# Performance work log

Measured on AMD Instinct MI355X. Metric: run time of the kernel, lower is better.

Reference implementation:

```python
import jax, jax.numpy as jnp
import numpy as np

BS = 8
LOW_RATIO = 0.25
HIGH_RATIO = 0.25


def _dct_matrix(n: int) -> np.ndarray:
    # DCT-II orthonormal matrix, row k = sqrt(2/n)*cos(pi*k*(2i+1)/(2n)), row 0 = 1/sqrt(n)
    k = np.arange(n)[:, None].astype(np.float64)
    i = np.arange(n)[None, :].astype(np.float64)
    D = np.sqrt(2.0 / n) * np.cos(np.pi * k * (2 * i + 1) / (2 * n))
    D[0, :] = 1.0 / np.sqrt(n)
    return D.astype(np.float32)


def _zigzag_indices(n: int) -> np.ndarray:
    idx = np.zeros((n, n), dtype=np.int64)
    i = j = 0
    for c in range(n * n):
        idx[i, j] = c
        if (i + j) % 2 == 0:
            if j == n - 1:
                i += 1
            elif i == 0:
                j += 1
            else:
                i -= 1; j += 1
        elif i == n - 1:
            j += 1
        elif j == 0:
            i += 1
        else:
            i += 1; j -= 1
    return idx


def _band_masks(n: int) -> np.ndarray:
    z = _zigzag_indices(n)
    total = n * n
    lo_thr = int(total * LOW_RATIO)        # 16 for n=8
    hi_thr = int(total * (1 - HIGH_RATIO)) # 48 for n=8
    low = (z < lo_thr)
    high = (z >= hi_thr)
    mid = ~(low | high)
    return np.stack([low, mid, high]).astype(np.float32)  # [3, n, n]


def setup_inputs() -> dict:
    key = jax.random.key(0)
    x = jax.random.normal(key, (32, 3, 512, 512), dtype=jnp.float32)
    return {"x": x}


def reference(x) -> jnp.ndarray:
    # Frequency decomposition: blocked 8x8 DCT -> band masking -> blocked IDCT.
    # Returns stacked (low, mid, high) bands: [3, B, C, H, W].
    D = jnp.asarray(_dct_matrix(BS))          # [bs, bs]
    M = jnp.asarray(_band_masks(BS))          # [3, bs, bs]
    B, C, H, W = x.shape
    Hb, Wb = H // BS, W // BS                 # H, W divisible by BS (no padding path)
    # blockify: [B, C, Hb, Wb, bs, bs]
    xb = x.reshape(B, C, Hb, BS, Wb, BS).transpose(0, 1, 2, 4, 3, 5)
    # forward block DCT: D @ block @ D^T
    coef = jnp.einsum('ki,bcuvij,lj->bcuvkl', D, xb, D)
    # band masking: [3, B, C, Hb, Wb, bs, bs]
    banded = coef[None] * M[:, None, None, None, None, :, :]
    # inverse block DCT: D^T @ coef @ D
    rec = jnp.einsum('ik,nbcuvkl,jl->nbcuvij', D, banded, D)
    # de-blockify back to images
    out = rec.transpose(0, 1, 2, 3, 5, 4, 6).reshape(3, B, C, H, W)
    return out
```

## Files before the change

kernel.cpp:

```cpp
#include <hip/hip_runtime.h>


namespace {

constexpr float DM[8][8] = {
  { 0.35355339059327373f, 0.35355339059327373f, 0.35355339059327373f, 0.35355339059327373f,
    0.35355339059327373f, 0.35355339059327373f, 0.35355339059327373f, 0.35355339059327373f },
  { 0.49039264020161522f, 0.41573480615127262f, 0.27778511650980114f, 0.09754516100806417f,
   -0.09754516100806417f,-0.27778511650980114f,-0.41573480615127262f,-0.49039264020161522f },
  { 0.46193976625564337f, 0.19134171618254492f,-0.19134171618254492f,-0.46193976625564337f,
   -0.46193976625564337f,-0.19134171618254492f, 0.19134171618254492f, 0.46193976625564337f },
  { 0.41573480615127262f,-0.09754516100806417f,-0.49039264020161522f,-0.27778511650980114f,
    0.27778511650980114f, 0.49039264020161522f, 0.09754516100806417f,-0.41573480615127262f },
  { 0.35355339059327373f,-0.35355339059327373f,-0.35355339059327373f, 0.35355339059327373f,
    0.35355339059327373f,-0.35355339059327373f,-0.35355339059327373f, 0.35355339059327373f },
  { 0.27778511650980114f,-0.49039264020161522f, 0.09754516100806417f, 0.41573480615127262f,
   -0.41573480615127262f,-0.09754516100806417f, 0.49039264020161522f,-0.27778511650980114f },
  { 0.19134171618254492f,-0.46193976625564337f, 0.46193976625564337f,-0.19134171618254492f,
   -0.19134171618254492f, 0.46193976625564337f,-0.46193976625564337f, 0.19134171618254492f },
  { 0.09754516100806417f,-0.27778511650980114f, 0.41573480615127262f,-0.49039264020161522f,
    0.49039264020161522f,-0.41573480615127262f, 0.27778511650980114f,-0.09754516100806417f }
};

constexpr int ZZ[8][8] = {
  { 0,  1,  5,  6, 14, 15, 27, 28},
  { 2,  4,  7, 13, 16, 26, 29, 42},
  { 3,  8, 12, 17, 25, 30, 41, 43},
  { 9, 11, 18, 24, 31, 40, 44, 53},
  {10, 19, 23, 32, 39, 45, 52, 54},
  {20, 22, 33, 38, 46, 51, 55, 60},
  {21, 34, 37, 47, 50, 56, 59, 61},
  {35, 36, 48, 49, 57, 58, 62, 63}
};

constexpr int band_of(int k, int l) {
  return ZZ[k][l] < 16 ? 0 : (ZZ[k][l] >= 48 ? 2 : 1);
}

}

__global__ __launch_bounds__(256) void freq_decomp_kernel(
    const float* __restrict__ x, float* __restrict__ out) {
  const int tid = blockIdx.x * 256 + threadIdx.x;
  const int wb = tid & 63;
  const int hb = (tid >> 6) & 63;
  const int bc = tid >> 12;

  const float* in = x + ((size_t)bc << 18) + (size_t)hb * 4096 + wb * 8;

  float X[8][8];
#pragma unroll
  for (int r = 0; r < 8; ++r) {
    const float4 a = *(const float4*)(in + (size_t)r * 512);
    const float4 b = *(const float4*)(in + (size_t)r * 512 + 4);
    X[r][0] = a.x; X[r][1] = a.y; X[r][2] = a.z; X[r][3] = a.w;
    X[r][4] = b.x; X[r][5] = b.y; X[r][6] = b.z; X[r][7] = b.w;
  }

  float V[8][8];
#pragma unroll
  for (int i = 0; i < 8; ++i) {
#pragma unroll
    for (int c = 0; c < 8; ++c) {
      float s = 0.0f;
#pragma unroll
      for (int j = 0; j < 8; ++j) s = fmaf(X[i][j], DM[c][j], s);
      V[i][c] = s;
    }
  }
  float T[8][8];
#pragma unroll
  for (int k = 0; k < 8; ++k) {
#pragma unroll
    for (int l = 0; l < 8; ++l) {
      float s = 0.0f;
#pragma unroll
      for (int i = 0; i < 8; ++i) s = fmaf(DM[k][i], V[i][l], s);
      T[k][l] = s;
    }
  }

  const size_t obase = ((size_t)bc << 18) + (size_t)hb * 4096 + wb * 8;

#pragma unroll
  for (int n = 0; n < 3; ++n) {
    float A[8][8];
#pragma unroll
    for (int i = 0; i < 8; ++i) {
#pragma unroll
      for (int l = 0; l < 8; ++l) {
        float s = 0.0f;
#pragma unroll
        for (int k = 0; k < 8; ++k) {
          if (band_of(k, l) == n) s = fmaf(DM[i][k], T[k][l], s);
        }
        A[i][l] = s;
      }
    }
    float* o = out + (size_t)n * 25165824 + obase;
#pragma unroll
    for (int i = 0; i < 8; ++i) {
      float y[8];
#pragma unroll
      for (int j = 0; j < 8; ++j) {
        float s = 0.0f;
#pragma unroll
        for (int l = 0; l < 8; ++l) s = fmaf(A[i][l], DM[j][l], s);
        y[j] = s;
      }
      *(float4*)(o + (size_t)i * 512)     = make_float4(y[0], y[1], y[2], y[3]);
      *(float4*)(o + (size_t)i * 512 + 4) = make_float4(y[4], y[5], y[6], y[7]);
    }
  }
}

extern "C" void kernel_launch(void* const* d_in, const int* in_sizes, int n_in,
                              void* d_out, int out_size, void* d_ws, size_t ws_size,
                              hipStream_t stream) {
  (void)in_sizes; (void)n_in; (void)d_ws; (void)ws_size; (void)out_size;
  const float* x = (const float*)d_in[0];
  float* out = (float*)d_out;
  const int total_threads = 32 * 3 * 64 * 64;
  freq_decomp_kernel<<<total_threads / 256, 256, 0, stream>>>(x, out);
}
```

Baseline: 371.9 us.

## Restructure DCT loops to cut live registers and skip zero band columns

The row DCT is now applied as each input row is loaded, and the inverse transform processes one output row at a time for all three bands together, so the full per-band intermediate matrices no longer stay live. It also sets a minimum-occupancy launch bound. The final column pass skips columns whose band mask is entirely zero, which drops FMAs that contribute nothing. The goal is lower register pressure and higher occupancy for this memory-bound kernel, at the cost of interleaving stores across three output planes.

```diff
diff --git a/kernel.cpp b/kernel.cpp
--- a/kernel.cpp
+++ b/kernel.cpp
@@ -39,78 +39,87 @@
 
 }
 
-__global__ __launch_bounds__(256) void freq_decomp_kernel(
+__global__ __launch_bounds__(256, 3) void freq_decomp_kernel(
     const float* __restrict__ x, float* __restrict__ out) {
   const int tid = blockIdx.x * 256 + threadIdx.x;
   const int wb = tid & 63;
   const int hb = (tid >> 6) & 63;
   const int bc = tid >> 12;
 
-  const float* in = x + ((size_t)bc << 18) + (size_t)hb * 4096 + wb * 8;
+  const size_t base = ((size_t)bc << 18) + (size_t)hb * 4096 + (size_t)(wb * 8);
+  const float* in = x + base;
 
-  float X[8][8];
+  float V[8][8];
 #pragma unroll
   for (int r = 0; r < 8; ++r) {
     const float4 a = *(const float4*)(in + (size_t)r * 512);
     const float4 b = *(const float4*)(in + (size_t)r * 512 + 4);
-    X[r][0] = a.x; X[r][1] = a.y; X[r][2] = a.z; X[r][3] = a.w;
-    X[r][4] = b.x; X[r][5] = b.y; X[r][6] = b.z; X[r][7] = b.w;
+    const float xr[8] = {a.x, a.y, a.z, a.w, b.x, b.y, b.z, b.w};
+#pragma unroll
+    for (int c = 0; c < 8; ++c) {
+      float s = xr[0] * DM[c][0];
+#pragma unroll
+      for (int j = 1; j < 8; ++j) s = fmaf(xr[j], DM[c][j], s);
+      V[r][c] = s;
+    }
   }
 
-  float V[8][8];
-#pragma unroll
-  for (int i = 0; i < 8; ++i) {
-#pragma unroll
-    for (int c = 0; c < 8; ++c) {
-      float s = 0.0f;
-#pragma unroll
-      for (int j = 0; j < 8; ++j) s = fmaf(X[i][j], DM[c][j], s);
-      V[i][c] = s;
-    }
-  }
   float T[8][8];
 #pragma unroll
-  for (int k = 0; k < 8; ++k) {
+  for (int l = 0; l < 8; ++l) {
 #pragma unroll
-    for (int l = 0; l < 8; ++l) {
-      float s = 0.0f;
+    for (int k = 0; k < 8; ++k) {
+      float s = DM[k][0] * V[0][l];
 #pragma unroll
-      for (int i = 0; i < 8; ++i) s = fmaf(DM[k][i], V[i][l], s);
+      for (int i = 1; i < 8; ++i) s = fmaf(DM[k][i], V[i][l], s);
       T[k][l] = s;
     }
   }
 
-  const size_t obase = ((size_t)bc << 18) + (size_t)hb * 4096 + wb * 8;
+  float* const olow  = out + base;
+  float* const omid  = olow + 25165824;
+  float* const ohigh = omid + 25165824;
 
 #pragma unroll
-  for (int n = 0; n < 3; ++n) {
-    float A[8][8];
+  for (int i = 0; i < 8; ++i) {
+    float AL[8], AM[8], AH[8];
 #pragma unroll
-    for (int i = 0; i < 8; ++i) {
+    for (int l = 0; l < 8; ++l) {
+      float sl = 0.0f, sm = 0.0f, sh = 0.0f;
 #pragma unroll
-      for (int l = 0; l < 8; ++l) {
-        float s = 0.0f;
+      for (int k = 0; k < 8; ++k) {
+        const int b = band_of(k, l);
+        if (b == 0) sl = fmaf(DM[i][k], T[k][l], sl);
+        else if (b == 1) sm = fmaf(DM[i][k], T[k][l], sm);
+        else sh = fmaf(DM[i][k], T[k][l], sh);
+      }
+      AL[l] = sl; AM[l] = sm; AH[l] = sh;
+    }
+
+    float yl[8], ym[8], yh[8];
 #pragma unroll
-        for (int k = 0; k < 8; ++k) {
-          if (band_of(k, l) == n) s = fmaf(DM[i][k], T[k][l], s);
-        }
-        A[i][l] = s;
-      }
+    for (int j = 0; j < 8; ++j) {
+      float s = AL[0] * DM[j][0];
+#pragma unroll
+      for (int l = 1; l < 6; ++l) s = fmaf(AL[l], DM[j][l], s);
+      yl[j] = s;
+      float t = AM[0] * DM[j][0];
+#pragma unroll
+      for (int l = 1; l < 8; ++l) t = fmaf(AM[l], DM[j][l], t);
+      ym[j] = t;
+      float u = AH[2] * DM[j][2];
+#pragma unroll
+      for (int l = 3; l < 8; ++l) u = fmaf(AH[l], DM[j][l], u);
+      yh[j] = u;
     }
-    float* o = out + (size_t)n * 25165824 + obase;
-#pragma unroll
-    for (int i = 0; i < 8; ++i) {
-      float y[8];
-#pragma unroll
-      for (int j = 0; j < 8; ++j) {
-        float s = 0.0f;
-#pragma unroll
-        for (int l = 0; l < 8; ++l) s = fmaf(A[i][l], DM[j][l], s);
-        y[j] = s;
-      }
-      *(float4*)(o + (size_t)i * 512)     = make_float4(y[0], y[1], y[2], y[3]);
-      *(float4*)(o + (size_t)i * 512 + 4) = make_float4(y[4], y[5], y[6], y[7]);
-    }
+
+    const size_t roff = (size_t)i * 512;
+    *(float4*)(olow  + roff)     = make_float4(yl[0], yl[1], yl[2], yl[3]);
+    *(float4*)(olow  + roff + 4) = make_float4(yl[4], yl[5], yl[6], yl[7]);
+    *(float4*)(omid  + roff)     = make_float4(ym[0], ym[1], ym[2], ym[3]);
+    *(float4*)(omid  + roff + 4) = make_float4(ym[4], ym[5], ym[6], ym[7]);
+    *(float4*)(ohigh + roff)     = make_float4(yh[0], yh[1], yh[2], yh[3]);
+    *(float4*)(ohigh + roff + 4) = make_float4(yh[4], yh[5], yh[6], yh[7]);
   }
 }
 
@@ -120,6 +129,5 @@
   (void)in_sizes; (void)n_in; (void)d_ws; (void)ws_size; (void)out_size;
   const float* x = (const float*)d_in[0];
   float* out = (float*)d_out;
-  const int total_threads = 32 * 3 * 64 * 64;
-  freq_decomp_kernel<<<total_threads / 256, 256, 0, stream>>>(x, out);
+  freq_decomp_kernel<<<1536, 256, 0, stream>>>(x, out);
 }
```

New measurement: 371.3 us. No clear change (-0.2%).
